# Performance work log

Measured on AMD Instinct MI355X. Metric: run time of the kernel, lower is better.

Reference implementation:

```python
import jax, jax.numpy as jnp
import numpy as np

E, TOPK, H, I, NSH = 8, 2, 2048, 5120, 2
B, S = 2, 1024


def setup_inputs() -> dict:
    key = jax.random.key(0)
    ks = jax.random.split(key, 8)
    sc = 0.02
    return {
        "x": jax.random.normal(ks[0], (B, S, H), dtype=jnp.float32),
        "w_router": jax.random.normal(ks[1], (E, H), dtype=jnp.float32),
        "wg": jax.random.normal(ks[2], (E, I, H), dtype=jnp.float32) * sc,
        "wu": jax.random.normal(ks[3], (E, I, H), dtype=jnp.float32) * sc,
        "wd": jax.random.normal(ks[4], (E, H, I), dtype=jnp.float32) * sc,
        "sg": jax.random.normal(ks[5], (NSH, I, H), dtype=jnp.float32) * sc,
        "su": jax.random.normal(ks[6], (NSH, I, H), dtype=jnp.float32) * sc,
        "sd": jax.random.normal(ks[7], (NSH, H, I), dtype=jnp.float32) * sc,
    }


def reference(x, w_router, wg, wu, wd, sg, su, sd):
    b, s, h = x.shape
    xt = x.reshape(-1, h)  # [T, H]
    T = xt.shape[0]

    # Router: fp32 linear, sigmoid scores, top-k, renormalize
    logits = jnp.einsum('th,eh->te', xt.astype(jnp.float32), w_router.astype(jnp.float32))
    scores = jax.nn.sigmoid(logits)
    topk_w, topk_i = jax.lax.top_k(scores, TOPK)
    topk_w = topk_w / jnp.sum(topk_w, axis=-1, keepdims=True)

    # Dense combine weights [T, E]: zero for non-selected experts
    comb = jnp.zeros((T, E), dtype=xt.dtype)
    comb = comb.at[jnp.arange(T)[:, None], topk_i].add(topk_w.astype(xt.dtype))

    # Routed experts (SwiGLU, no bias): compute all, combine with sparse weights
    gate = jax.nn.silu(jnp.einsum('th,eih->tei', xt, wg))
    up = jnp.einsum('th,eih->tei', xt, wu)
    expert_out = jnp.einsum('tei,ehi->teh', gate * up, wd)
    out = jnp.einsum('te,teh->th', comb, expert_out)

    # Shared experts: applied to every token, summed
    sgate = jax.nn.silu(jnp.einsum('th,jih->tji', xt, sg))
    sup = jnp.einsum('th,jih->tji', xt, su)
    out = out + jnp.einsum('tji,jhi->th', sgate * sup, sd)

    return out.reshape(b, s, h)
```

## Files before the change

### kernel.cpp

```cpp
#include <hip/hip_runtime.h>
#include <stdint.h>


#define E_ 8
#define H_ 2048
#define I_ 5120
#define T_ 2048
#define NSLOT 10

typedef __attribute__((ext_vector_type(4))) float f32x4;
typedef __attribute__((ext_vector_type(8))) __bf16 bf16x8;
typedef __attribute__((ext_vector_type(4))) unsigned int u32x4;
typedef __attribute__((ext_vector_type(2))) unsigned int u32x2;

__device__ __forceinline__ int sw(int r) { return (r ^ (r >> 2)) & 3; }

typedef __attribute__((address_space(1))) const void* gptr1_t;
typedef __attribute__((address_space(3))) void* lptr3_t;
__device__ __forceinline__ void load_lds16(const void* g, void* l) {
  __builtin_amdgcn_global_load_lds((gptr1_t)g, (lptr3_t)l, 16, 0, 0);
}

#define PIPE_SYNC(N)                                                    \
  do {                                                                  \
    asm volatile("s_waitcnt vmcnt(" #N ") lgkmcnt(0)" ::: "memory");    \
    __builtin_amdgcn_sched_barrier(0);                                  \
    __builtin_amdgcn_s_barrier();                                       \
    __builtin_amdgcn_sched_barrier(0);                                  \
  } while (0)

__device__ __forceinline__ unsigned short f2bf(float f) {
  unsigned u = __builtin_bit_cast(unsigned, f);
  u += 0x7FFFu + ((u >> 16) & 1u);
  return (unsigned short)(u >> 16);
}

__device__ __forceinline__ u32x2 cvt4(f32x4 v) {
  unsigned r0, r1;
  asm("v_cvt_pk_bf16_f32 %0, %1, %2" : "=v"(r0) : "v"(v[0]), "v"(v[1]));
  asm("v_cvt_pk_bf16_f32 %0, %1, %2" : "=v"(r1) : "v"(v[2]), "v"(v[3]));
  u32x2 w; w[0] = r0; w[1] = r1;
  return w;
}

__global__ __launch_bounds__(256) void k_castx(const float* __restrict__ x,
                                               unsigned short* __restrict__ xb) {
  const int i = (blockIdx.x * 256 + threadIdx.x) * 8;
  f32x4 a = *(const f32x4*)(x + i);
  f32x4 b = *(const f32x4*)(x + i + 4);
  u32x2 lo = cvt4(a), hi = cvt4(b);
  u32x4 o; o[0] = lo[0]; o[1] = lo[1]; o[2] = hi[0]; o[3] = hi[1];
  *(u32x4*)(xb + i) = o;
}

__global__ __launch_bounds__(64) void k_router(const float* __restrict__ x,
                                               const float* __restrict__ wr,
                                               int* __restrict__ tki,
                                               float* __restrict__ tkw) {
  const int t = blockIdx.x, lane = threadIdx.x;
  const float* xr = x + (size_t)t * H_;
  float lg[E_];
#pragma unroll
  for (int e = 0; e < E_; ++e) {
    const float* w = wr + (size_t)e * H_;
    float acc = 0.f;
    for (int k = lane; k < H_; k += 64) acc += xr[k] * w[k];
#pragma unroll
    for (int off = 32; off > 0; off >>= 1) acc += __shfl_down(acc, off);
    lg[e] = acc;
  }
  if (lane == 0) {
    float sc[E_];
#pragma unroll
    for (int e = 0; e < E_; ++e) sc[e] = 1.f / (1.f + expf(-lg[e]));
    int b0 = 0;
#pragma unroll
    for (int e = 1; e < E_; ++e) if (sc[e] > sc[b0]) b0 = e;
    int b1 = -1;
#pragma unroll
    for (int e = 0; e < E_; ++e) {
      if (e == b0) continue;
      if (b1 < 0 || sc[e] > sc[b1]) b1 = e;
    }
    float s0 = sc[b0], s1 = sc[b1], inv = 1.f / (s0 + s1);
    tki[2 * t] = b0; tki[2 * t + 1] = b1;
    tkw[2 * t] = s0 * inv; tkw[2 * t + 1] = s1 * inv;
  }
}

__global__ __launch_bounds__(64) void k_lists(const int* __restrict__ tki,
                                              const float* __restrict__ tkw,
                                              int* __restrict__ elist,
                                              float* __restrict__ ew,
                                              int* __restrict__ ecnt,
                                              int* __restrict__ ipos) {
  const int s = blockIdx.x, lane = threadIdx.x;
  if (s < E_) {
    int base = 0;
    for (int c = 0; c < T_ / 64; ++c) {
      int t = c * 64 + lane;
      int i0 = tki[2 * t], i1 = tki[2 * t + 1];
      int flag = (i0 == s) ? 1 : ((i1 == s) ? 2 : 0);
      unsigned long long m = __ballot(flag != 0);
      int pre = __popcll(m & ((1ull << lane) - 1ull));
      if (flag) {
        elist[s * T_ + base + pre] = t;
        ew[s * T_ + base + pre] = tkw[2 * t + flag - 1];
        ipos[2 * t + flag - 1] = base + pre;
      }
      base += __popcll(m);
    }
    int padded = (base + 255) & ~255;
    for (int p = base + lane; p < padded; p += 64) { elist[s * T_ + p] = 0; ew[s * T_ + p] = 0.f; }
    if (lane == 0) ecnt[s] = base;
  } else {
    for (int i = lane; i < T_; i += 64) { elist[s * T_ + i] = i; ew[s * T_ + i] = 1.f; }
    if (lane == 0) ecnt[s] = T_;
  }
}

__global__ void k_bases(const int* __restrict__ ecnt, int* __restrict__ sbase) {
  if (threadIdx.x == 0 && blockIdx.x == 0) {
    int b = 0;
    for (int s = 0; s < NSLOT; ++s) { sbase[s] = b; b += (ecnt[s] + 255) & ~255; }
  }
}

__global__ __launch_bounds__(1024, 4) void k_gateup(
    const unsigned short* __restrict__ xb,
    const float* __restrict__ wg_all, const float* __restrict__ wu_all,
    const float* __restrict__ sg_all, const float* __restrict__ su_all,
    const int* __restrict__ elist, const float* __restrict__ ew,
    const int* __restrict__ ecnt,
    const int* __restrict__ sbase, unsigned short* __restrict__ h) {
  const int s = blockIdx.z;
  const int cnt = ecnt[s];
  const int r0 = blockIdx.y * 256;
  if (r0 >= cnt) return;
  const int n0 = blockIdx.x * 128;
  const float* gw; const float* uw;
  if (s < E_) { gw = wg_all + (size_t)s * I_ * H_; uw = wu_all + (size_t)s * I_ * H_; }
  else        { gw = sg_all + (size_t)(s - E_) * I_ * H_; uw = su_all + (size_t)(s - E_) * I_ * H_; }
  const int* lst = elist + s * T_;
  const int hrow0 = sbase[s] + r0;

  __shared__ u32x4 sA[3][1024];
  __shared__ u32x4 sG[2][512];
  __shared__ u32x4 sU[2][512];

  const int tid = threadIdx.x;
  const int wv = tid >> 6, lane = tid & 63;
  const int wr = wv >> 2, wc = wv & 3;
  const int fr = lane & 15, k8 = lane >> 4;

  const int arow = wv * 16 + (lane >> 2);
  int li = r0 + arow; if (li >= cnt) li = r0;
  const unsigned short* aSrc =
      xb + (size_t)lst[li] * H_ + (((lane & 3) ^ sw(arow)) * 8);

  const int br = tid >> 3, cb = (tid & 7) >> 1, bh = tid & 1;
  const float* gp = gw + (size_t)(n0 + br) * H_ + (tid & 7) * 4;
  const float* up = uw + (size_t)(n0 + br) * H_ + (tid & 7) * 4;
  f32x4 rg, ru;

  f32x4 accg[4][2], accu[4][2];
#pragma unroll
  for (int m = 0; m < 4; ++m)
#pragma unroll
    for (int n = 0; n < 2; ++n) {
      accg[m][n] = (f32x4){0.f, 0.f, 0.f, 0.f};
      accu[m][n] = (f32x4){0.f, 0.f, 0.f, 0.f};
    }

  auto dmaA = [&](int b, int kt) {
    load_lds16(aSrc + kt * 32, &sA[b][wv * 64]);
  };
  auto loadB = [&]() {
    rg = *(const f32x4*)gp; ru = *(const f32x4*)up;
    gp += 32; up += 32;
  };
  auto stageB = [&](int b) {
    ((u32x2*)&sG[b][br * 4 + (cb ^ sw(br))])[bh] = cvt4(rg);
    ((u32x2*)&sU[b][br * 4 + (cb ^ sw(br))])[bh] = cvt4(ru);
  };
  auto compute = [&](int a, int b) {
    bf16x8 af[4], gf[2], uf[2];
#pragma unroll
    for (int m = 0; m < 4; ++m) {
      int r = wr * 64 + m * 16 + fr;
      af[m] = __builtin_bit_cast(bf16x8, sA[a][r * 4 + (k8 ^ sw(r))]);
    }
#pragma unroll
    for (int n = 0; n < 2; ++n) {
      int r = wc * 32 + n * 16 + fr;
      gf[n] = __builtin_bit_cast(bf16x8, sG[b][r * 4 + (k8 ^ sw(r))]);
      uf[n] = __builtin_bit_cast(bf16x8, sU[b][r * 4 + (k8 ^ sw(r))]);
    }
#pragma unroll
    for (int m = 0; m < 4; ++m)
#pragma unroll
      for (int n = 0; n < 2; ++n) {
        accg[m][n] = __builtin_amdgcn_mfma_f32_16x16x32_bf16(af[m], gf[n], accg[m][n], 0, 0, 0);
        accu[m][n] = __builtin_amdgcn_mfma_f32_16x16x32_bf16(af[m], uf[n], accu[m][n], 0, 0, 0);
      }
  };

  const int KT = H_ / 32;
  loadB();
  dmaA(0, 0);
  stageB(0);
  loadB();
  dmaA(1, 1);
  PIPE_SYNC(3);
  int aCur = 0, bCur = 0;
  for (int kt = 0; kt < KT; ++kt) {
    compute(aCur, bCur);
    if (kt + 1 < KT) {
      stageB(bCur ^ 1);
      if (kt + 2 < KT) {
        int nx = aCur + 2; if (nx >= 3) nx -= 3;
        dmaA(nx, kt + 2);
        loadB();
        PIPE_SYNC(3);
      } else {
        PIPE_SYNC(0);
      }
      aCur = (aCur == 2) ? 0 : aCur + 1;
      bCur ^= 1;
    }
  }

#pragma unroll
  for (int m = 0; m < 4; ++m)
#pragma unroll
    for (int r = 0; r < 4; ++r) {
      int rit = wr * 64 + m * 16 + k8 * 4 + r;
      if (r0 + rit < cnt) {
        float wgt = ew[s * T_ + r0 + rit];
        unsigned short* hrow = h + (size_t)(hrow0 + rit) * I_ + n0 + wc * 32;
#pragma unroll
        for (int n = 0; n < 2; ++n) {
          float g = accg[m][n][r], uv = accu[m][n][r];
          float hv = g / (1.f + expf(-g)) * uv * wgt;
          hrow[n * 16 + fr] = f2bf(hv);
        }
      }
    }
}

__global__ __launch_bounds__(512, 4) void k_down(
    const unsigned short* __restrict__ h,
    const float* __restrict__ wd_all, const float* __restrict__ sd_all,
    const int* __restrict__ elist,
    const int* __restrict__ ecnt, const int* __restrict__ sbase,
    float* __restrict__ y, int use_y,
    float* __restrict__ out) {
  const int s = blockIdx.z;
  const int cnt = ecnt[s];
  const int r0 = blockIdx.y * 256;
  if (r0 >= cnt) return;
  const int n0 = blockIdx.x * 128;
  const float* bw = (s < E_) ? wd_all + (size_t)s * H_ * I_
                             : sd_all + (size_t)(s - E_) * H_ * I_;
  const int hrow0 = sbase[s] + r0;

  __shared__ u32x4 sA[3][1024];
  __shared__ u32x4 sB[2][512];

  const int tid = threadIdx.x;
  const int wv = tid >> 6, lane = tid & 63;
  const int wr = wv >> 1, wc = wv & 1;
  const int fr = lane & 15, k8 = lane >> 4;

  const int arow0 = wv * 32 + (lane >> 2);
  const int arow1 = arow0 + 16;
  const unsigned short* aSrc0 =
      h + (size_t)(hrow0 + arow0) * I_ + (((lane & 3) ^ sw(arow0)) * 8);
  const unsigned short* aSrc1 =
      h + (size_t)(hrow0 + arow1) * I_ + (((lane & 3) ^ sw(arow1)) * 8);

  const int brr = tid >> 2, cb = tid & 3;
  const float* bp = bw + (size_t)(n0 + brr) * I_ + cb * 8;
  f32x4 rb0, rb1;

  f32x4 acc[4][4];
#pragma unroll
  for (int m = 0; m < 4; ++m)
#pragma unroll
    for (int n = 0; n < 4; ++n) acc[m][n] = (f32x4){0.f, 0.f, 0.f, 0.f};

  auto dmaA = [&](int b, int kt) {
    load_lds16(aSrc0 + kt * 32, &sA[b][wv * 128]);
    load_lds16(aSrc1 + kt * 32, &sA[b][wv * 128 + 64]);
  };
  auto loadB = [&]() {
    rb0 = *(const f32x4*)bp; rb1 = *(const f32x4*)(bp + 4); bp += 32;
  };
  auto stageB = [&](int b) {
    u32x2 lo = cvt4(rb0), hi = cvt4(rb1);
    u32x4 q; q[0] = lo[0]; q[1] = lo[1]; q[2] = hi[0]; q[3] = hi[1];
    sB[b][brr * 4 + (cb ^ sw(brr))] = q;
  };
  auto compute = [&](int a, int b) {
    bf16x8 af[4], bf[4];
#pragma unroll
    for (int m = 0; m < 4; ++m) {
      int r = wr * 64 + m * 16 + fr;
      af[m] = __builtin_bit_cast(bf16x8, sA[a][r * 4 + (k8 ^ sw(r))]);
    }
#pragma unroll
    for (int n = 0; n < 4; ++n) {
      int r = wc * 64 + n * 16 + fr;
      bf[n] = __builtin_bit_cast(bf16x8, sB[b][r * 4 + (k8 ^ sw(r))]);
    }
#pragma unroll
    for (int m = 0; m < 4; ++m)
#pragma unroll
      for (int n = 0; n < 4; ++n)
        acc[m][n] = __builtin_amdgcn_mfma_f32_16x16x32_bf16(af[m], bf[n], acc[m][n], 0, 0, 0);
  };

  const int KT = I_ / 32;
  loadB();
  dmaA(0, 0);
  stageB(0);
  loadB();
  dmaA(1, 1);
  PIPE_SYNC(4);
  int aCur = 0, bCur = 0;
  for (int kt = 0; kt < KT; ++kt) {
    compute(aCur, bCur);
    if (kt + 1 < KT) {
      stageB(bCur ^ 1);
      if (kt + 2 < KT) {
        int nx = aCur + 2; if (nx >= 3) nx -= 3;
        dmaA(nx, kt + 2);
        loadB();
        PIPE_SYNC(4);
      } else {
        PIPE_SYNC(0);
      }
      aCur = (aCur == 2) ? 0 : aCur + 1;
      bCur ^= 1;
    }
  }

  if (use_y) {
#pragma unroll
    for (int m = 0; m < 4; ++m)
#pragma unroll
      for (int r = 0; r < 4; ++r) {
        int rit = wr * 64 + m * 16 + k8 * 4 + r;
        float* yrow = y + (size_t)(hrow0 + rit) * H_ + n0 + wc * 64 + fr;
#pragma unroll
        for (int n = 0; n < 4; ++n) yrow[n * 16] = acc[m][n][r];
      }
  } else {
    const int* lst = elist + s * T_;
#pragma unroll
    for (int m = 0; m < 4; ++m)
#pragma unroll
      for (int r = 0; r < 4; ++r) {
        int rit = wr * 64 + m * 16 + k8 * 4 + r;
        if (r0 + rit < cnt) {
          int t = lst[r0 + rit];
          float* orow = out + (size_t)t * H_ + n0 + wc * 64 + fr;
#pragma unroll
          for (int n = 0; n < 4; ++n) atomicAdd(orow + n * 16, acc[m][n][r]);
        }
      }
  }
}

__global__ __launch_bounds__(256) void k_combine(
    const float* __restrict__ y, const int* __restrict__ tki,
    const int* __restrict__ ipos, const int* __restrict__ sbase,
    float* __restrict__ out) {
  const int t = blockIdx.x;
  const int c = threadIdx.x * 8;
  const size_t r0 = (size_t)(sbase[tki[2 * t]] + ipos[2 * t]) * H_ + c;
  const size_t r1 = (size_t)(sbase[tki[2 * t + 1]] + ipos[2 * t + 1]) * H_ + c;
  const size_t r2 = (size_t)(sbase[8] + t) * H_ + c;
  const size_t r3 = (size_t)(sbase[9] + t) * H_ + c;
  f32x4 a0 = *(const f32x4*)(y + r0), b0 = *(const f32x4*)(y + r0 + 4);
  f32x4 a1 = *(const f32x4*)(y + r1), b1 = *(const f32x4*)(y + r1 + 4);
  f32x4 a2 = *(const f32x4*)(y + r2), b2 = *(const f32x4*)(y + r2 + 4);
  f32x4 a3 = *(const f32x4*)(y + r3), b3 = *(const f32x4*)(y + r3 + 4);
  f32x4 sa = (a0 + a1) + (a2 + a3);
  f32x4 sb = (b0 + b1) + (b2 + b3);
  float* o = out + (size_t)t * H_ + c;
  *(f32x4*)o = sa;
  *(f32x4*)(o + 4) = sb;
}

extern "C" void kernel_launch(void* const* d_in, const int* in_sizes, int n_in,
                              void* d_out, int out_size, void* d_ws, size_t ws_size,
                              hipStream_t stream) {
  const float* x  = (const float*)d_in[0];
  const float* wr = (const float*)d_in[1];
  const float* wg = (const float*)d_in[2];
  const float* wu = (const float*)d_in[3];
  const float* wd = (const float*)d_in[4];
  const float* sg = (const float*)d_in[5];
  const float* su = (const float*)d_in[6];
  const float* sd = (const float*)d_in[7];
  float* out = (float*)d_out;
  char* ws = (char*)d_ws;

  int*   tki   = (int*)(ws);
  float* tkw   = (float*)(ws + 16384);
  int*   elist = (int*)(ws + 32768);
  float* ew    = (float*)(ws + 114688);
  int*   ecnt  = (int*)(ws + 196608);
  int*   sbase = (int*)(ws + 196864);
  int*   ipos  = (int*)(ws + 197632);
  unsigned short* xb = (unsigned short*)(ws + 262144);
  unsigned short* h  = (unsigned short*)(ws + 262144 + 8388608);
  float* y = (float*)(ws + 262144 + 8388608 + 107479040);
  const size_t ws_need_y = 262144ull + 8388608ull + 107479040ull + 85983232ull;
  const int use_y = (ws_size >= ws_need_y) ? 1 : 0;

  k_castx<<<T_ * H_ / (256 * 8), 256, 0, stream>>>(x, xb);
  k_router<<<T_, 64, 0, stream>>>(x, wr, tki, tkw);
  k_lists<<<NSLOT, 64, 0, stream>>>(tki, tkw, elist, ew, ecnt, ipos);
  k_bases<<<1, 1, 0, stream>>>(ecnt, sbase);
  k_gateup<<<dim3(I_ / 128, T_ / 256, NSLOT), 1024, 0, stream>>>(
      xb, wg, wu, sg, su, elist, ew, ecnt, sbase, h);
  if (!use_y) hipMemsetAsync(out, 0, (size_t)T_ * H_ * sizeof(float), stream);
  k_down<<<dim3(H_ / 128, T_ / 256, NSLOT), 512, 0, stream>>>(
      h, wd, sd, elist, ecnt, sbase, y, use_y, out);
  if (use_y)
    k_combine<<<T_, 256, 0, stream>>>(y, tki, ipos, sbase, out);
}
```

Baseline: 969.5 us.

## Shrink gate/up tile to 128 rows and use register-staged double buffering

The gate/up kernel drops from 1024-thread blocks covering a 256x128 output tile to 512-thread blocks covering a 128x128 tile, doubling the grid along the token dimension. The async global-to-LDS DMA for activations and the 3-stage pipeline are replaced by plain register loads for activations and both weight matrices, staged into a simple 2-buffer LDS ring with __syncthreads. The aim is smaller blocks, less LDS and simpler synchronisation for better occupancy. The cost is that each fp32 weight tile is now read and converted twice as often, and there is less latency hiding than the DMA-based pipeline gave.

```diff
diff --git a/kernel.cpp b/kernel.cpp
--- a/kernel.cpp
+++ b/kernel.cpp
@@ -126,7 +126,7 @@
   }
 }
 
-__global__ __launch_bounds__(1024, 4) void k_gateup(
+__global__ __launch_bounds__(512, 4) void k_gateup(
     const unsigned short* __restrict__ xb,
     const float* __restrict__ wg_all, const float* __restrict__ wu_all,
     const float* __restrict__ sg_all, const float* __restrict__ su_all,
@@ -135,7 +135,7 @@
     const int* __restrict__ sbase, unsigned short* __restrict__ h) {
   const int s = blockIdx.z;
   const int cnt = ecnt[s];
-  const int r0 = blockIdx.y * 256;
+  const int r0 = blockIdx.y * 128;
   if (r0 >= cnt) return;
   const int n0 = blockIdx.x * 128;
   const float* gw; const float* uw;
@@ -144,24 +144,23 @@
   const int* lst = elist + s * T_;
   const int hrow0 = sbase[s] + r0;
 
-  __shared__ u32x4 sA[3][1024];
-  __shared__ u32x4 sG[2][512];
-  __shared__ u32x4 sU[2][512];
+  __shared__ u32x4 sA[2][128 * 4];
+  __shared__ u32x4 sG[2][128 * 4];
+  __shared__ u32x4 sU[2][128 * 4];
 
   const int tid = threadIdx.x;
   const int wv = tid >> 6, lane = tid & 63;
   const int wr = wv >> 2, wc = wv & 3;
   const int fr = lane & 15, k8 = lane >> 4;
 
-  const int arow = wv * 16 + (lane >> 2);
-  int li = r0 + arow; if (li >= cnt) li = r0;
-  const unsigned short* aSrc =
-      xb + (size_t)lst[li] * H_ + (((lane & 3) ^ sw(arow)) * 8);
-
-  const int br = tid >> 3, cb = (tid & 7) >> 1, bh = tid & 1;
-  const float* gp = gw + (size_t)(n0 + br) * H_ + (tid & 7) * 4;
-  const float* up = uw + (size_t)(n0 + br) * H_ + (tid & 7) * 4;
-  f32x4 rg, ru;
+  const int ar = tid >> 2, ca = tid & 3;
+  int li = r0 + ar; if (li >= cnt) li = r0;
+  const unsigned short* xp = xb + (size_t)lst[li] * H_ + ca * 8;
+  const int br = tid >> 2, cb = tid & 3;
+  const float* gp = gw + (size_t)(n0 + br) * H_ + cb * 8;
+  const float* up = uw + (size_t)(n0 + br) * H_ + cb * 8;
+
+  u32x4 ra; f32x4 rg0, rg1, ru0, ru1;
 
   f32x4 accg[4][2], accu[4][2];
 #pragma unroll
@@ -172,23 +171,27 @@
       accu[m][n] = (f32x4){0.f, 0.f, 0.f, 0.f};
     }
 
-  auto dmaA = [&](int b, int kt) {
-    load_lds16(aSrc + kt * 32, &sA[b][wv * 64]);
-  };
-  auto loadB = [&]() {
-    rg = *(const f32x4*)gp; ru = *(const f32x4*)up;
-    gp += 32; up += 32;
-  };
-  auto stageB = [&](int b) {
-    ((u32x2*)&sG[b][br * 4 + (cb ^ sw(br))])[bh] = cvt4(rg);
-    ((u32x2*)&sU[b][br * 4 + (cb ^ sw(br))])[bh] = cvt4(ru);
-  };
-  auto compute = [&](int a, int b) {
+  auto loadNext = [&]() {
+    ra = *(const u32x4*)xp;
+    rg0 = *(const f32x4*)gp; rg1 = *(const f32x4*)(gp + 4);
+    ru0 = *(const f32x4*)up; ru1 = *(const f32x4*)(up + 4);
+    xp += 32; gp += 32; up += 32;
+  };
+  auto stage = [&](int b) {
+    sA[b][ar * 4 + (ca ^ sw(ar))] = ra;
+    u32x2 glo = cvt4(rg0), ghi = cvt4(rg1);
+    u32x4 gq; gq[0] = glo[0]; gq[1] = glo[1]; gq[2] = ghi[0]; gq[3] = ghi[1];
+    sG[b][br * 4 + (cb ^ sw(br))] = gq;
+    u32x2 ulo = cvt4(ru0), uhi = cvt4(ru1);
+    u32x4 uq; uq[0] = ulo[0]; uq[1] = ulo[1]; uq[2] = uhi[0]; uq[3] = uhi[1];
+    sU[b][br * 4 + (cb ^ sw(br))] = uq;
+  };
+  auto compute = [&](int b) {
     bf16x8 af[4], gf[2], uf[2];
 #pragma unroll
     for (int m = 0; m < 4; ++m) {
       int r = wr * 64 + m * 16 + fr;
-      af[m] = __builtin_bit_cast(bf16x8, sA[a][r * 4 + (k8 ^ sw(r))]);
+      af[m] = __builtin_bit_cast(bf16x8, sA[b][r * 4 + (k8 ^ sw(r))]);
     }
 #pragma unroll
     for (int n = 0; n < 2; ++n) {
@@ -206,27 +209,18 @@
   };
 
   const int KT = H_ / 32;
-  loadB();
-  dmaA(0, 0);
-  stageB(0);
-  loadB();
-  dmaA(1, 1);
-  PIPE_SYNC(3);
-  int aCur = 0, bCur = 0;
+  loadNext();
+  stage(0);
+  loadNext();
+  __syncthreads();
+  int cur = 0;
   for (int kt = 0; kt < KT; ++kt) {
-    compute(aCur, bCur);
+    compute(cur);
     if (kt + 1 < KT) {
-      stageB(bCur ^ 1);
-      if (kt + 2 < KT) {
-        int nx = aCur + 2; if (nx >= 3) nx -= 3;
-        dmaA(nx, kt + 2);
-        loadB();
-        PIPE_SYNC(3);
-      } else {
-        PIPE_SYNC(0);
-      }
-      aCur = (aCur == 2) ? 0 : aCur + 1;
-      bCur ^= 1;
+      stage(cur ^ 1);
+      if (kt + 2 < KT) loadNext();
+      __syncthreads();
+      cur ^= 1;
     }
   }
 
@@ -424,7 +418,7 @@
   k_router<<<T_, 64, 0, stream>>>(x, wr, tki, tkw);
   k_lists<<<NSLOT, 64, 0, stream>>>(tki, tkw, elist, ew, ecnt, ipos);
   k_bases<<<1, 1, 0, stream>>>(ecnt, sbase);
-  k_gateup<<<dim3(I_ / 128, T_ / 256, NSLOT), 1024, 0, stream>>>(
+  k_gateup<<<dim3(I_ / 128, T_ / 128, NSLOT), 512, 0, stream>>>(
       xb, wg, wu, sg, su, elist, ew, ecnt, sbase, h);
   if (!use_y) hipMemsetAsync(out, 0, (size_t)T_ * H_ * sizeof(float), stream);
   k_down<<<dim3(H_ / 128, T_ / 256, NSLOT), 512, 0, stream>>>(
```

New measurement: 1.107 ms. 14.2% more time.
